# Kernel optimization log

Measured on AMD Instinct MI355X. Metric: run time of the kernel, lower is better.

Reference implementation:

```python
import jax, jax.numpy as jnp
import numpy as np

L1, L2 = 16, 16            # lattice shape -> translation group
N_SYMM = L1 * L2           # 256 group elements
IN_FEATURES = 32
FEATURES = 64
BATCH = 16


def translation_table(l1, l2):
    """Product table pt[g, h] = index of g^{-1} h for the 2D translation group."""
    n = l1 * l2
    g = np.arange(n)
    a, b = g // l2, g % l2          # coords of g
    c, d = a, b                     # coords of h (same enumeration)
    pt = ((c[None, :] - a[:, None]) % l1) * l2 + ((d[None, :] - b[:, None]) % l2)
    return jnp.asarray(pt, dtype=jnp.int32)  # (n_symm, n_symm)


def setup_inputs() -> dict:
    key = jax.random.key(0)
    kx, kk, kb = jax.random.split(key, 3)
    x = jax.random.normal(kx, (BATCH, IN_FEATURES, N_SYMM), dtype=jnp.float32)
    # default_equivariant_initializer ~ lecun normal, fan_in = in_features * kernel_size
    scale = 1.0 / np.sqrt(IN_FEATURES * N_SYMM)
    kernel = scale * jax.random.normal(kk, (FEATURES, IN_FEATURES, N_SYMM), dtype=jnp.float32)
    bias = jnp.zeros((FEATURES,), dtype=jnp.float32)
    product_table = translation_table(L1, L2)
    return {"x": x, "kernel": kernel, "bias": bias, "product_table": product_table}


def reference(x, kernel, bias, product_table):
    # Expand kernel via group product table: K[f, i, g, h] = kernel[f, i, pt[g, h]]
    # (feature_group_count = 1, mask = None so unmask is identity, kernel_size = n_symm)
    K = jnp.take(kernel, product_table, axis=2)          # (F, I, S, S) -- 536 MB fp32
    # dot_general contracts x dims (in_features, n_symm) with K dims (I, first S)
    out = jnp.einsum('big,figh->bfh', x, K)              # (B, F, S)
    out = out + bias[:, None]                            # bias broadcast over group dim
    return out
```

## Files before the change

### kernel.cpp

```cpp
#include <hip/hip_runtime.h>

typedef unsigned short u16;
typedef unsigned int u32;
typedef __attribute__((ext_vector_type(8))) short bfx8;
typedef __attribute__((ext_vector_type(4))) float fx4;
typedef __attribute__((ext_vector_type(4))) u32 ux4;
typedef __attribute__((ext_vector_type(2))) u32 ux2;

#define KELEMS (64 * 32 * 256)
#define XELEMS (16 * 32 * 256)
#define WS1_OFFB (KELEMS * 2)
#define WS2_OFFB (WS1_OFFB + XELEMS * 2)

__device__ inline u16 f2bf(float v) {
  u32 u = __builtin_bit_cast(u32, v);
  u = (u + 0x7fffu + ((u >> 16) & 1u)) >> 16;
  return (u16)u;
}

__global__ __launch_bounds__(256) void eq_convert(const float* __restrict__ kin,
                                                  const float* __restrict__ xin,
                                                  u16* __restrict__ kbf,
                                                  u16* __restrict__ xbf) {
  int e = (blockIdx.x * 256 + threadIdx.x) * 4;
  if (e < KELEMS) {
    fx4 v = *(const fx4*)(kin + e);
    int f = e >> 13, i = (e >> 8) & 31, s = e & 255;
    int o = ((i << 6) + f) * 256 + s;
    ux2 p;
    p[0] = (u32)f2bf(v[0]) | ((u32)f2bf(v[1]) << 16);
    p[1] = (u32)f2bf(v[2]) | ((u32)f2bf(v[3]) << 16);
    *(ux2*)(kbf + o) = p;
  } else {
    int ex = e - KELEMS;
    fx4 v = *(const fx4*)(xin + ex);
    ux2 p;
    p[0] = (u32)f2bf(v[0]) | ((u32)f2bf(v[1]) << 16);
    p[1] = (u32)f2bf(v[2]) | ((u32)f2bf(v[3]) << 16);
    *(ux2*)(xbf + ex) = p;
  }
}

__global__ __launch_bounds__(256, 2) void eq_main(const u16* __restrict__ kbf,
                                                  const u16* __restrict__ xbf,
                                                  float* __restrict__ part) {
  __shared__ u16 As[16384];
  __shared__ u16 xraw[256];
  __shared__ u32 P[512];

  const int bid = blockIdx.x;
  const int b = bid & 15;
  const int i = bid >> 4;
  const int t = threadIdx.x;

  const u16* ks = kbf + i * 16384;
#pragma unroll
  for (int it = 0; it < 8; ++it) {
    int slot = it * 256 + t;
    int f = slot >> 5;
    int c = (slot & 31) ^ (f & 31);
    ux4 v = *(const ux4*)(ks + f * 256 + c * 8);
    *(ux4*)(As + slot * 8) = v;
  }
  if (t < 64) {
    ux2 v = *(const ux2*)(xbf + ((b << 5) + i) * 256 + t * 4);
    *(ux2*)(xraw + t * 4) = v;
  }
  __syncthreads();

  {
    int r = t >> 4, u = t & 15;
    int c0 = (32 - 2 * u) & 15;
    int c1 = (c0 + 15) & 15;
    int c2 = (c0 + 14) & 15;
    u32 va = xraw[r * 16 + c0];
    u32 vb = xraw[r * 16 + c1];
    u32 vc = xraw[r * 16 + c2];
    P[r * 32 + u] = va | (vb << 16);
    P[r * 32 + 16 + u] = vb | (vc << 16);
  }
  __syncthreads();

  const int lane = t & 63;
  const int w = t >> 6;
  const int n = lane & 15;
  const int quad = lane >> 4;
  const int s2_0 = (quad & 1) << 3;
  const int par = n & 1;
  const int u0 = ((s2_0 - n - par) & 15) >> 1;
  const int Pb = (par << 4) + u0;
  const int s1q = quad >> 1;

  fx4 acc[4][4];
#pragma unroll
  for (int a = 0; a < 4; ++a)
#pragma unroll
    for (int c = 0; c < 4; ++c) acc[a][c] = (fx4){0.f, 0.f, 0.f, 0.f};

#pragma unroll
  for (int kstep = 0; kstep < 8; ++kstep) {
    bfx8 af[4];
#pragma unroll
    for (int ft = 0; ft < 4; ++ft) {
      int f = (ft << 4) + n;
      int ch = ((kstep << 2) + quad) ^ (f & 31);
      af[ft] = *(const bfx8*)(As + f * 256 + ch * 8);
    }
    const int s1 = (kstep << 1) + s1q;
    bfx8 bfr[4];
#pragma unroll
    for (int ht = 0; ht < 4; ++ht) {
      int r = ((w << 2) + ht - s1) & 15;
      int idx = r * 32 + Pb;
      ux4 bv = {P[idx], P[idx + 1], P[idx + 2], P[idx + 3]};
      bfr[ht] = __builtin_bit_cast(bfx8, bv);
    }
#pragma unroll
    for (int ft = 0; ft < 4; ++ft)
#pragma unroll
      for (int ht = 0; ht < 4; ++ht)
        acc[ft][ht] =
            __builtin_amdgcn_mfma_f32_16x16x32_bf16(af[ft], bfr[ht], acc[ft][ht], 0, 0, 0);
  }

  float* pw = part + (((i << 4) + b) << 14);
#pragma unroll
  for (int ft = 0; ft < 4; ++ft) {
#pragma unroll
    for (int reg = 0; reg < 4; ++reg) {
      int f = (ft << 4) + (quad << 2) + reg;
#pragma unroll
      for (int ht = 0; ht < 4; ++ht) {
        int h = (w << 6) + (ht << 4) + n;
        pw[f * 256 + h] = acc[ft][ht][reg];
      }
    }
  }
}

__global__ __launch_bounds__(256) void eq_reduce(const float* __restrict__ part,
                                                 const float* __restrict__ bias,
                                                 float* __restrict__ out) {
  int o = (blockIdx.x * 256 + threadIdx.x) * 4;
  fx4 s = {0.f, 0.f, 0.f, 0.f};
#pragma unroll
  for (int i = 0; i < 32; ++i) s = s + *(const fx4*)(part + i * 262144 + o);
  float bv = bias[(o >> 8) & 63];
  s = s + (fx4){bv, bv, bv, bv};
  *(fx4*)(out + o) = s;
}

extern "C" void kernel_launch(void* const* d_in, const int* in_sizes, int n_in,
                              void* d_out, int out_size, void* d_ws, size_t ws_size,
                              hipStream_t stream) {
  (void)in_sizes; (void)n_in; (void)out_size; (void)ws_size;
  const float* x = (const float*)d_in[0];
  const float* k = (const float*)d_in[1];
  const float* bias = (const float*)d_in[2];
  u16* kbf = (u16*)((char*)d_ws);
  u16* xbf = (u16*)((char*)d_ws + WS1_OFFB);
  float* part = (float*)((char*)d_ws + WS2_OFFB);
  float* out = (float*)d_out;

  eq_convert<<<640, 256, 0, stream>>>(k, x, kbf, xbf);
  eq_main<<<512, 256, 0, stream>>>(kbf, xbf, part);
  eq_reduce<<<256, 256, 0, stream>>>(part, bias, out);
}
```

Before: 80.07 us.

## Fuse bf16 conversion into main kernel and pair input channels per block

```diff
diff --git a/kernel.cpp b/kernel.cpp
--- a/kernel.cpp
+++ b/kernel.cpp
@@ -7,89 +7,77 @@
 typedef __attribute__((ext_vector_type(4))) u32 ux4;
 typedef __attribute__((ext_vector_type(2))) u32 ux2;
 
-#define KELEMS (64 * 32 * 256)
-#define XELEMS (16 * 32 * 256)
-#define WS1_OFFB (KELEMS * 2)
-#define WS2_OFFB (WS1_OFFB + XELEMS * 2)
-
-__device__ inline u16 f2bf(float v) {
+__device__ inline u32 f2bf(float v) {
   u32 u = __builtin_bit_cast(u32, v);
   u = (u + 0x7fffu + ((u >> 16) & 1u)) >> 16;
-  return (u16)u;
+  return u;
 }
 
-__global__ __launch_bounds__(256) void eq_convert(const float* __restrict__ kin,
-                                                  const float* __restrict__ xin,
-                                                  u16* __restrict__ kbf,
-                                                  u16* __restrict__ xbf) {
-  int e = (blockIdx.x * 256 + threadIdx.x) * 4;
-  if (e < KELEMS) {
-    fx4 v = *(const fx4*)(kin + e);
-    int f = e >> 13, i = (e >> 8) & 31, s = e & 255;
-    int o = ((i << 6) + f) * 256 + s;
-    ux2 p;
-    p[0] = (u32)f2bf(v[0]) | ((u32)f2bf(v[1]) << 16);
-    p[1] = (u32)f2bf(v[2]) | ((u32)f2bf(v[3]) << 16);
-    *(ux2*)(kbf + o) = p;
-  } else {
-    int ex = e - KELEMS;
-    fx4 v = *(const fx4*)(xin + ex);
-    ux2 p;
-    p[0] = (u32)f2bf(v[0]) | ((u32)f2bf(v[1]) << 16);
-    p[1] = (u32)f2bf(v[2]) | ((u32)f2bf(v[3]) << 16);
-    *(ux2*)(xbf + ex) = p;
-  }
-}
+__global__ __launch_bounds__(512, 1) void eq_main(const float* __restrict__ xin,
+                                                  const float* __restrict__ kin,
+                                                  float* __restrict__ part) {
+  __shared__ u16 As[32768];
+  __shared__ u32 P[1024];
+  __shared__ u16 xraw[512];
+  __shared__ float red[4 * 64 * 68];
 
-__global__ __launch_bounds__(256, 2) void eq_main(const u16* __restrict__ kbf,
-                                                  const u16* __restrict__ xbf,
-                                                  float* __restrict__ part) {
-  __shared__ u16 As[16384];
-  __shared__ u16 xraw[256];
-  __shared__ u32 P[512];
-
-  const int bid = blockIdx.x;
-  const int b = bid & 15;
-  const int i = bid >> 4;
+  const int b = blockIdx.x & 15;
+  const int ich = blockIdx.x >> 4;
   const int t = threadIdx.x;
 
-  const u16* ks = kbf + i * 16384;
+  if (t < 128) {
+    int iLoc = t >> 6, s4 = (t & 63) << 2;
+    fx4 v = *(const fx4*)(xin + ((b << 5) + (ich << 1) + iLoc) * 256 + s4);
+    ux2 p;
+    p[0] = f2bf(v[0]) | (f2bf(v[1]) << 16);
+    p[1] = f2bf(v[2]) | (f2bf(v[3]) << 16);
+    *(ux2*)(xraw + iLoc * 256 + s4) = p;
+  }
+
 #pragma unroll
   for (int it = 0; it < 8; ++it) {
-    int slot = it * 256 + t;
-    int f = slot >> 5;
-    int c = (slot & 31) ^ (f & 31);
-    ux4 v = *(const ux4*)(ks + f * 256 + c * 8);
-    *(ux4*)(As + slot * 8) = v;
-  }
-  if (t < 64) {
-    ux2 v = *(const ux2*)(xbf + ((b << 5) + i) * 256 + t * 4);
-    *(ux2*)(xraw + t * 4) = v;
+    int slot = it * 512 + t;
+    int iLoc = slot >> 11;
+    int f = (slot >> 5) & 63;
+    int c = slot & 31;
+    int cs = c ^ (f & 31);
+    const float* src = kin + f * 8192 + ((ich << 1) + iLoc) * 256 + (cs << 3);
+    fx4 v0 = *(const fx4*)src;
+    fx4 v1 = *(const fx4*)(src + 4);
+    ux4 p;
+    p[0] = f2bf(v0[0]) | (f2bf(v0[1]) << 16);
+    p[1] = f2bf(v0[2]) | (f2bf(v0[3]) << 16);
+    p[2] = f2bf(v1[0]) | (f2bf(v1[1]) << 16);
+    p[3] = f2bf(v1[2]) | (f2bf(v1[3]) << 16);
+    *(ux4*)(As + slot * 8) = p;
   }
   __syncthreads();
 
   {
-    int r = t >> 4, u = t & 15;
+    int iLoc = t >> 8, tt = t & 255;
+    int r = tt >> 4, u = tt & 15;
     int c0 = (32 - 2 * u) & 15;
     int c1 = (c0 + 15) & 15;
     int c2 = (c0 + 14) & 15;
-    u32 va = xraw[r * 16 + c0];
-    u32 vb = xraw[r * 16 + c1];
-    u32 vc = xraw[r * 16 + c2];
-    P[r * 32 + u] = va | (vb << 16);
-    P[r * 32 + 16 + u] = vb | (vc << 16);
+    const u16* xr = xraw + iLoc * 256 + r * 16;
+    u32 va = xr[c0], vb = xr[c1], vc = xr[c2];
+    P[iLoc * 512 + r * 32 + u] = va | (vb << 16);
+    P[iLoc * 512 + r * 32 + 16 + u] = vb | (vc << 16);
   }
   __syncthreads();
 
   const int lane = t & 63;
   const int w = t >> 6;
+  const int iLoc = w >> 2;
+  const int wq = w & 3;
   const int n = lane & 15;
   const int quad = lane >> 4;
   const int s2_0 = (quad & 1) << 3;
   const int par = n & 1;
   const int u0 = ((s2_0 - n - par) & 15) >> 1;
-  const int Pb = (par << 4) + u0;
+  const int Pb = iLoc * 512 + (par << 4) + u0;
   const int s1q = quad >> 1;
+  const u16* Aw = As + (iLoc << 14);
 
   fx4 acc[4][4];
 #pragma unroll
@@ -104,13 +92,13 @@
     for (int ft = 0; ft < 4; ++ft) {
       int f = (ft << 4) + n;
       int ch = ((kstep << 2) + quad) ^ (f & 31);
-      af[ft] = *(const bfx8*)(As + f * 256 + ch * 8);
+      af[ft] = *(const bfx8*)(Aw + f * 256 + ch * 8);
     }
     const int s1 = (kstep << 1) + s1q;
     bfx8 bfr[4];
 #pragma unroll
     for (int ht = 0; ht < 4; ++ht) {
-      int r = ((w << 2) + ht - s1) & 15;
+      int r = ((wq << 2) + ht - s1) & 15;
       int idx = r * 32 + Pb;
       ux4 bv = {P[idx], P[idx + 1], P[idx + 2], P[idx + 3]};
       bfr[ht] = __builtin_bit_cast(bfx8, bv);
@@ -123,18 +111,32 @@
             __builtin_amdgcn_mfma_f32_16x16x32_bf16(af[ft], bfr[ht], acc[ft][ht], 0, 0, 0);
   }
 
-  float* pw = part + (((i << 4) + b) << 14);
+  if (w >= 4) {
 #pragma unroll
-  for (int ft = 0; ft < 4; ++ft) {
-#pragma unroll
-    for (int reg = 0; reg < 4; ++reg) {
-      int f = (ft << 4) + (quad << 2) + reg;
+    for (int ft = 0; ft < 4; ++ft)
 #pragma unroll
       for (int ht = 0; ht < 4; ++ht) {
-        int h = (w << 6) + (ht << 4) + n;
-        pw[f * 256 + h] = acc[ft][ht][reg];
+        float* pr = &red[wq * 4352 + (ht * 16 + n) * 68 + (ft << 4) + (quad << 2)];
+        *(fx4*)pr = acc[ft][ht];
       }
-    }
+  }
+  __syncthreads();
+  if (w < 4) {
+    float* pw = part + (((ich << 4) + b) << 14);
+#pragma unroll
+    for (int ft = 0; ft < 4; ++ft)
+#pragma unroll
+      for (int ht = 0; ht < 4; ++ht) {
+        const float* pr = &red[wq * 4352 + (ht * 16 + n) * 68 + (ft << 4) + (quad << 2)];
+        fx4 vv = *(const fx4*)pr;
+        acc[ft][ht] = acc[ft][ht] + vv;
+#pragma unroll
+        for (int reg = 0; reg < 4; ++reg) {
+          int f = (ft << 4) + (quad << 2) + reg;
+          int h = (wq << 6) + (ht << 4) + n;
+          pw[f * 256 + h] = acc[ft][ht][reg];
+        }
+      }
   }
 }
 
@@ -144,7 +146,7 @@
   int o = (blockIdx.x * 256 + threadIdx.x) * 4;
   fx4 s = {0.f, 0.f, 0.f, 0.f};
 #pragma unroll
-  for (int i = 0; i < 32; ++i) s = s + *(const fx4*)(part + i * 262144 + o);
+  for (int i = 0; i < 16; ++i) s = s + *(const fx4*)(part + i * 262144 + o);
   float bv = bias[(o >> 8) & 63];
   s = s + (fx4){bv, bv, bv, bv};
   *(fx4*)(out + o) = s;
@@ -157,12 +159,9 @@
   const float* x = (const float*)d_in[0];
   const float* k = (const float*)d_in[1];
   const float* bias = (const float*)d_in[2];
-  u16* kbf = (u16*)((char*)d_ws);
-  u16* xbf = (u16*)((char*)d_ws + WS1_OFFB);
-  float* part = (float*)((char*)d_ws + WS2_OFFB);
+  float* part = (float*)d_ws;
   float* out = (float*)d_out;
 
-  eq_convert<<<640, 256, 0, stream>>>(k, x, kbf, xbf);
-  eq_main<<<512, 256, 0, stream>>>(kbf, xbf, part);
+  eq_main<<<256, 512, 0, stream>>>(x, k, part);
   eq_reduce<<<256, 256, 0, stream>>>(part, bias, out);
 }
```

Measured after the change: 73.46 us. -8.3%, faster.
